# Kernel optimization log

Hardware: AMD Instinct MI355X
Metric: run time of the kernel (lower is better)

The kernel has to match this reference:

```python
import jax, jax.numpy as jnp
import numpy as np

B, K = 16, 256
APP, DK, DG, NR = 768, 96, 96, 8


def setup_inputs() -> dict:
    key = jax.random.key(0)
    ks = jax.random.split(key, 10)
    sA = 1.0 / np.sqrt(APP)  # torch Linear default init scale
    sG = 1.0 / np.sqrt(DG)
    return {
        "f_a": jax.random.normal(ks[0], (B, K, APP), jnp.float32),
        "position_embedding": jax.random.uniform(ks[1], (B, K, K, DG), jnp.float32),
        "WG_w": jax.random.normal(ks[2], (NR, DG), jnp.float32) * sG,
        "WG_b": jnp.zeros((NR,), jnp.float32),
        "WK_w": jax.random.normal(ks[3], (NR, DK, APP), jnp.float32) * sA,
        "WK_b": jnp.zeros((NR, DK), jnp.float32),
        "WQ_w": jax.random.normal(ks[4], (NR, DK, APP), jnp.float32) * sA,
        "WQ_b": jnp.zeros((NR, DK), jnp.float32),
        "WV_w": jax.random.normal(ks[5], (NR, DK, APP), jnp.float32) * sA,
        "WV_b": jnp.zeros((NR, DK), jnp.float32),
    }


def reference(f_a, position_embedding, WG_w, WG_b, WK_w, WK_b, WQ_w, WQ_b, WV_w, WV_b):
    # geometric bias: [NR, B, K, K]
    w_g = jax.nn.relu(jnp.einsum('bmng,rg->rbmn', position_embedding, WG_w)
                      + WG_b[:, None, None, None])
    # projections: [NR, B, K, DK]
    w_k = jnp.einsum('bmd,rkd->rbmk', f_a, WK_w) + WK_b[:, None, None, :]
    w_q = jnp.einsum('bnd,rkd->rbnk', f_a, WQ_w) + WQ_b[:, None, None, :]
    w_v = jnp.einsum('bmd,rkd->rbmk', f_a, WV_w) + WV_b[:, None, None, :]
    # scaled dot: scores[r,b,m,n] = <k_m, q_n>/sqrt(DK)
    scores = jnp.einsum('rbmk,rbnk->rbmn', w_k, w_q) / jnp.sqrt(jnp.float32(DK))
    logits = jnp.log(jnp.clip(w_g, 1e-6)) + scores
    # softmax over m (the key index, torch dim=1 of [B,K,K])
    att = jax.nn.softmax(logits, axis=2)
    # out[r,b,n,k] = sum_m att[r,b,m,n] * v[r,b,m,k]
    out = jnp.einsum('rbmn,rbmk->rbnk', att, w_v)
    # concat units along feature dim -> [B, K, NR*DK], residual add
    out = out.transpose(1, 2, 0, 3).reshape(B, K, NR * DK)
    return out + f_a
```

## Files before the change

### kernel.cpp

```cpp
#include <hip/hip_runtime.h>
#include <hip/hip_bf16.h>

typedef __attribute__((ext_vector_type(8))) short s16x8;
typedef __attribute__((ext_vector_type(4))) float f32x4;
typedef unsigned short u16;
typedef unsigned int u32;

#define NB 16
#define NK 256
#define APP 768
#define DKK 96
#define NR 8
#define QSCALE 0.10206207261596575f

__device__ __forceinline__ u16 f2bf(float f) {
  union { float f; unsigned int u; } v; v.f = f;
  unsigned int x = v.u;
  x += 0x7fffu + ((x >> 16) & 1u);
  return (u16)(x >> 16);
}
__device__ __forceinline__ float bf2f(u16 h) {
  union { unsigned int u; float f; } v; v.u = ((unsigned int)h) << 16;
  return v.f;
}
__device__ __forceinline__ u32 cvtpk(float lo, float hi) {
  u32 r;
  asm("v_cvt_pk_bf16_f32 %0, %1, %2" : "=v"(r) : "v"(lo), "v"(hi));
  return r;
}
__device__ __forceinline__ float bflo(u32 pk) {
  union { u32 u; float f; } v; v.u = pk << 16; return v.f;
}
__device__ __forceinline__ float bfhi(u32 pk) {
  union { u32 u; float f; } v; v.u = pk & 0xffff0000u; return v.f;
}
__device__ __forceinline__ void gload_lds16(const void* g, void* l) {
  __builtin_amdgcn_global_load_lds(
      (const __attribute__((address_space(1))) unsigned int*)g,
      (__attribute__((address_space(3))) unsigned int*)l, 16, 0, 0);
}

__global__ __launch_bounds__(256) void conv_kernel(
    const float* __restrict__ fa,
    const float* __restrict__ WKw, const float* __restrict__ WQw,
    const float* __restrict__ WVw,
    u16* __restrict__ fab, u16* __restrict__ Wb)
{
  const int idx = blockIdx.x * 256 + threadIdx.x;
  const int faCh = NB * NK * APP / 8;
  const int wCh  = NR * DKK * APP / 8;
  const float* src; u16* dst;
  if (idx < faCh) {
    src = fa + (size_t)idx * 8;
    dst = fab + (size_t)idx * 8;
  } else {
    int o = idx - faCh;
    int a = o / wCh;
    int oo = o - a * wCh;
    const float* wsrc = a == 0 ? WKw : (a == 1 ? WQw : WVw);
    src = wsrc + (size_t)oo * 8;
    dst = Wb + (size_t)a * (NR * DKK * APP) + (size_t)oo * 8;
  }
  float4 v0 = *(const float4*)src;
  float4 v1 = *(const float4*)(src + 4);
  s16x8 ov = {(short)f2bf(v0.x),(short)f2bf(v0.y),(short)f2bf(v0.z),(short)f2bf(v0.w),
              (short)f2bf(v1.x),(short)f2bf(v1.y),(short)f2bf(v1.z),(short)f2bf(v1.w)};
  *(s16x8*)dst = ov;
}

#define PROJ_BLKS 576
#define WG_BLKS 8192

__global__ __launch_bounds__(256) void fused_kernel(
    const u16* __restrict__ fab, const u16* __restrict__ Wb,
    const float* __restrict__ WKb, const float* __restrict__ WQb,
    const float* __restrict__ WVb,
    u16* __restrict__ wkF, u16* __restrict__ wqF, u16* __restrict__ wvF,
    const float* __restrict__ pos,
    const float* __restrict__ WGw, const float* __restrict__ WGb,
    u16* __restrict__ lb2)
{
  __shared__ u16 SH[26624];
  const int t = threadIdx.x;
  const int lane = t & 63, w = t >> 6;
  const int c = lane & 15, g = lane >> 4;
  const int bid = blockIdx.x;
  const int q = bid / 15, rph = bid - q * 15;

  if (rph == 0 && q < PROJ_BLKS) {
    u16* As = SH;
    u16* Bs = SH + 8192;
    const int pb = q;
    const int wr = w >> 1, wc = w & 1;
    const int m0 = (pb & 31) * 128;
    const int ct = pb >> 5;
    const int c0 = ct * 128;

    f32x4 acc[4][4] = {};

    for (int k0 = 0; k0 < APP; k0 += 64) {
      __syncthreads();
      #pragma unroll
      for (int i = 0; i < 4; ++i) {
        int n = t + i * 256;
        int row = n >> 3, cg = n & 7;
        int scg = cg ^ (row & 7);
        gload_lds16(fab + (size_t)(m0 + row) * APP + k0 + scg * 8, As + n * 8);
        gload_lds16(Wb  + (size_t)(c0 + row) * APP + k0 + scg * 8, Bs + n * 8);
      }
      __syncthreads();
      #pragma unroll
      for (int kc = 0; kc < 2; ++kc) {
        s16x8 af[4], bfr[4];
        #pragma unroll
        for (int i = 0; i < 4; ++i) {
          int arow = wr * 64 + i * 16 + c;
          af[i]  = *(const s16x8*)(As + (((arow << 3) | ((kc * 4 + g) ^ (arow & 7))) << 3));
          int brow = wc * 64 + i * 16 + c;
          bfr[i] = *(const s16x8*)(Bs + (((brow << 3) | ((kc * 4 + g) ^ (brow & 7))) << 3));
        }
        #pragma unroll
        for (int mi = 0; mi < 4; ++mi)
          #pragma unroll
          for (int ni = 0; ni < 4; ++ni)
            acc[mi][ni] = __builtin_amdgcn_mfma_f32_16x16x32_bf16(af[mi], bfr[ni], acc[mi][ni], 0, 0, 0);
      }
    }

    const int arr = ct / 6;
    const int cw0 = c0 - arr * APP;
    const float* bp = arr == 0 ? WKb : (arr == 1 ? WQb : WVb);

    #pragma unroll
    for (int mi = 0; mi < 4; ++mi)
      #pragma unroll
      for (int ni = 0; ni < 4; ++ni) {
        int clw = cw0 + wc * 64 + ni * 16 + c;
        float bias = bp[clw];
        int rr = clw / DKK, kk = clw - rr * DKK;
        int mb = m0 + wr * 64 + mi * 16 + g * 4;
        int bi = mb >> 8, tt = mb & 255;
        size_t hb = (size_t)rr * NB + bi;
        if (arr == 2) {
          ushort4 pk4;
          pk4.x = f2bf(acc[mi][ni][0] + bias);
          pk4.y = f2bf(acc[mi][ni][1] + bias);
          pk4.z = f2bf(acc[mi][ni][2] + bias);
          pk4.w = f2bf(acc[mi][ni][3] + bias);
          *(ushort4*)&wvF[((hb * 32 + (tt >> 3)) * DKK + kk) * 8 + (tt & 7)] = pk4;
        } else {
          u16* op = arr == 0 ? wkF : wqF;
          size_t base = ((hb * 12 + (kk >> 3)) * NK) * 8 + (size_t)(kk & 7);
          #pragma unroll
          for (int e = 0; e < 4; ++e) {
            float val = acc[mi][ni][e] + bias;
            if (arr == 1) val *= QSCALE;
            op[base + (size_t)(tt + e) * 8] = f2bf(val);
          }
        }
      }
  } else {
    const int nbefore = (q >= PROJ_BLKS) ? PROJ_BLKS : (q + (rph > 0 ? 1 : 0));
    const int wgid = bid - nbefore;
    u16* Th = SH;
    u16* Tl = SH + 13312;
    const size_t row0 = (size_t)wgid * 128;

    s16x8 bwh[3], bwl[3];
    #pragma unroll
    for (int kc = 0; kc < 3; ++kc) {
      const float* wp = WGw + (c & 7) * DKK + kc * 32 + g * 8;
      s16x8 hv, lv;
      #pragma unroll
      for (int j = 0; j < 4; ++j) {
        float x0 = wp[2 * j], x1 = wp[2 * j + 1];
        u32 h = cvtpk(x0, x1);
        u32 l = cvtpk(x0 - bflo(h), x1 - bfhi(h));
        hv[2 * j] = (short)(h & 0xffff); hv[2 * j + 1] = (short)(h >> 16);
        lv[2 * j] = (short)(l & 0xffff); lv[2 * j + 1] = (short)(l >> 16);
      }
      bwh[kc] = hv; bwl[kc] = lv;
    }
    const float bias = WGb[c & 7];

    #pragma unroll
    for (int i = 0; i < 6; ++i) {
      int qq = t + i * 256;
      int row = qq / 12, col8 = qq - row * 12;
      const float* s = pos + row0 * DKK + (size_t)qq * 8;
      float4 a = *(const float4*)s;
      float4 b = *(const float4*)(s + 4);
      uint4 ph, pl;
      ph.x = cvtpk(a.x, a.y); pl.x = cvtpk(a.x - bflo(ph.x), a.y - bfhi(ph.x));
      ph.y = cvtpk(a.z, a.w); pl.y = cvtpk(a.z - bflo(ph.y), a.w - bfhi(ph.y));
      ph.z = cvtpk(b.x, b.y); pl.z = cvtpk(b.x - bflo(ph.z), b.y - bfhi(ph.z));
      ph.w = cvtpk(b.z, b.w); pl.w = cvtpk(b.z - bflo(ph.w), b.w - bfhi(ph.w));
      *(uint4*)&Th[row * 104 + col8 * 8] = ph;
      *(uint4*)&Tl[row * 104 + col8 * 8] = pl;
    }
    __syncthreads();

    #pragma unroll
    for (int gi = 0; gi < 2; ++gi) {
      int rowl = w * 32 + gi * 16;
      f32x4 acc = {0.f, 0.f, 0.f, 0.f};
      #pragma unroll
      for (int kc = 0; kc < 3; ++kc) {
        s16x8 ah = *(const s16x8*)&Th[(rowl + c) * 104 + kc * 32 + g * 8];
        s16x8 al = *(const s16x8*)&Tl[(rowl + c) * 104 + kc * 32 + g * 8];
        acc = __builtin_amdgcn_mfma_f32_16x16x32_bf16(ah, bwh[kc], acc, 0, 0, 0);
        acc = __builtin_amdgcn_mfma_f32_16x16x32_bf16(ah, bwl[kc], acc, 0, 0, 0);
        acc = __builtin_amdgcn_mfma_f32_16x16x32_bf16(al, bwh[kc], acc, 0, 0, 0);
      }
      if (c < 8) {
        size_t base = (size_t)c * (NB * NK * NK) + row0 + rowl + g * 4;
        float v0 = __logf(fmaxf(acc[0] + bias, 1e-6f));
        float v1 = __logf(fmaxf(acc[1] + bias, 1e-6f));
        float v2 = __logf(fmaxf(acc[2] + bias, 1e-6f));
        float v3 = __logf(fmaxf(acc[3] + bias, 1e-6f));
        uint2 pk;
        pk.x = cvtpk(v0, v1);
        pk.y = cvtpk(v2, v3);
        *(uint2*)(lb2 + base) = pk;
      }
    }
  }
}

__global__ __launch_bounds__(256) void attn_kernel(
    const u16* __restrict__ wkF, const u16* __restrict__ wqF,
    const u16* __restrict__ wvF, const u16* __restrict__ lb2,
    const float* __restrict__ fa, float* __restrict__ out)
{
  __shared__ u16 Ps[4][16][40];
  const int t = threadIdx.x;
  const int w = t >> 6, lane = t & 63;
  const int c = lane & 15, g = lane >> 4;
  const int b = blockIdx.y, r = blockIdx.z;
  const int nb = blockIdx.x * 64 + w * 16;

  const size_t hb = (size_t)r * NB + b;
  const u16* Qb = wqF + hb * (12 * NK * 8);
  const u16* Kb = wkF + hb * (12 * NK * 8);
  const u16* Vb = wvF + hb * (32 * DKK * 8);
  const u16* Br = lb2 + hb * NK * NK + (size_t)c * NK + nb + g * 4;

  s16x8 qf[3];
  #pragma unroll
  for (int kc = 0; kc < 3; ++kc)
    qf[kc] = *(const s16x8*)(Qb + ((kc * 4 + g) * NK + nb + c) * 8);

  ushort4 bbr[16];
  #pragma unroll
  for (int mt = 0; mt < 16; ++mt)
    bbr[mt] = *(const ushort4*)(Br + (size_t)mt * 16 * NK);

  f32x4 S[16];
  #pragma unroll
  for (int mt = 0; mt < 16; ++mt) {
    f32x4 sa = {bf2f(bbr[mt].x), bf2f(bbr[mt].y), bf2f(bbr[mt].z), bf2f(bbr[mt].w)};
    #pragma unroll
    for (int kc = 0; kc < 3; ++kc) {
      s16x8 kf = *(const s16x8*)(Kb + ((kc * 4 + g) * NK + mt * 16 + c) * 8);
      sa = __builtin_amdgcn_mfma_f32_16x16x32_bf16(qf[kc], kf, sa, 0, 0, 0);
    }
    S[mt] = sa;
  }

  float rinv[4];
  #pragma unroll
  for (int e = 0; e < 4; ++e) {
    float mx = S[0][e];
    #pragma unroll
    for (int mt = 1; mt < 16; ++mt) mx = fmaxf(mx, S[mt][e]);
    mx = fmaxf(mx, __shfl_xor(mx, 1));
    mx = fmaxf(mx, __shfl_xor(mx, 2));
    mx = fmaxf(mx, __shfl_xor(mx, 4));
    mx = fmaxf(mx, __shfl_xor(mx, 8));
    float sm = 0.f;
    #pragma unroll
    for (int mt = 0; mt < 16; ++mt) {
      float p = __expf(S[mt][e] - mx);
      S[mt][e] = p;
      sm += p;
    }
    sm += __shfl_xor(sm, 1);
    sm += __shfl_xor(sm, 2);
    sm += __shfl_xor(sm, 4);
    sm += __shfl_xor(sm, 8);
    rinv[e] = 1.f / sm;
  }

  f32x4 o[6];
  #pragma unroll
  for (int ki = 0; ki < 6; ++ki) o[ki] = (f32x4){0.f, 0.f, 0.f, 0.f};

  #pragma unroll
  for (int mc = 0; mc < 8; ++mc) {
    #pragma unroll
    for (int e = 0; e < 4; ++e) {
      Ps[w][g * 4 + e][c]      = f2bf(S[2 * mc][e]);
      Ps[w][g * 4 + e][16 + c] = f2bf(S[2 * mc + 1][e]);
    }
    s16x8 pa = *(const s16x8*)&Ps[w][c][g * 8];
    #pragma unroll
    for (int ki = 0; ki < 6; ++ki) {
      s16x8 vf = *(const s16x8*)(Vb + ((mc * 4 + g) * DKK + ki * 16 + c) * 8);
      o[ki] = __builtin_amdgcn_mfma_f32_16x16x32_bf16(pa, vf, o[ki], 0, 0, 0);
    }
  }

  #pragma unroll
  for (int ki = 0; ki < 6; ++ki)
    #pragma unroll
    for (int e = 0; e < 4; ++e) {
      int n = nb + g * 4 + e;
      size_t adr = ((size_t)b * NK + n) * (NR * DKK) + r * DKK + ki * 16 + c;
      out[adr] = o[ki][e] * rinv[e] + fa[adr];
    }
}

extern "C" void kernel_launch(void* const* d_in, const int* in_sizes, int n_in,
                              void* d_out, int out_size, void* d_ws, size_t ws_size,
                              hipStream_t stream) {
  (void)in_sizes; (void)n_in; (void)out_size; (void)ws_size;
  const float* fa  = (const float*)d_in[0];
  const float* pos = (const float*)d_in[1];
  const float* WGw = (const float*)d_in[2];
  const float* WGb = (const float*)d_in[3];
  const float* WKw = (const float*)d_in[4];
  const float* WKb = (const float*)d_in[5];
  const float* WQw = (const float*)d_in[6];
  const float* WQb = (const float*)d_in[7];
  const float* WVw = (const float*)d_in[8];
  const float* WVb = (const float*)d_in[9];
  float* outp = (float*)d_out;

  const size_t faN = (size_t)NB * NK * APP;
  const size_t wN  = (size_t)3 * NR * DKK * APP;
  const size_t kqv = (size_t)NR * NB * NK * DKK;
  u16* fab = (u16*)d_ws;
  u16* Wb  = fab + faN;
  u16* wkF = Wb + wN;
  u16* wqF = wkF + kqv;
  u16* wvF = wqF + kqv;
  u16* lb2 = wvF + kqv;

  hipLaunchKernelGGL(conv_kernel, dim3(2400), dim3(256), 0, stream,
                     fa, WKw, WQw, WVw, fab, Wb);
  hipLaunchKernelGGL(fused_kernel, dim3(PROJ_BLKS + WG_BLKS), dim3(256), 0, stream,
                     fab, Wb, WKb, WQb, WVb, wkF, wqF, wvF, pos, WGw, WGb, lb2);
  hipLaunchKernelGGL(attn_kernel, dim3(4, NB, NR), dim3(256), 0, stream,
                     wkF, wqF, wvF, lb2, fa, outp);
}
```

Measured before the change: 137.4 us.

## Make geometric-bias blocks persistent with double-buffered register prefetch

The geometric-bias part of the fused kernel now uses 2304 persistent blocks that loop over 16384 tiles of 64 rows, instead of 8192 one-shot blocks of 128 rows. Each iteration prefetches the next tile's position embeddings into registers while the MFMA work on the current LDS buffer runs, then writes the split bf16 hi/lo values into the other LDS buffer. The interleave with projection blocks changes from one in every 15 blocks to one in every 5, for 2880 blocks total. The aim is to hide global load latency on the memory-bound position-embedding stream and cut block launch overhead, at the cost of more live registers and a barrier on every tile.

Result: no change. 134.8 us (-1.8%).

```diff
diff --git a/kernel.cpp b/kernel.cpp
--- a/kernel.cpp
+++ b/kernel.cpp
@@ -69,7 +69,8 @@
 }
 
 #define PROJ_BLKS 576
-#define WG_BLKS 8192
+#define WG_BLKS 2304
+#define NTILES 16384
 
 __global__ __launch_bounds__(256) void fused_kernel(
     const u16* __restrict__ fab, const u16* __restrict__ Wb,
@@ -85,9 +86,9 @@
   const int lane = t & 63, w = t >> 6;
   const int c = lane & 15, g = lane >> 4;
   const int bid = blockIdx.x;
-  const int q = bid / 15, rph = bid - q * 15;
-
-  if (rph == 0 && q < PROJ_BLKS) {
+  const int q = bid / 5, rem = bid - q * 5;
+
+  if (rem == 0) {
     u16* As = SH;
     u16* Bs = SH + 8192;
     const int pb = q;
@@ -160,11 +161,7 @@
         }
       }
   } else {
-    const int nbefore = (q >= PROJ_BLKS) ? PROJ_BLKS : (q + (rph > 0 ? 1 : 0));
-    const int wgid = bid - nbefore;
-    u16* Th = SH;
-    u16* Tl = SH + 13312;
-    const size_t row0 = (size_t)wgid * 128;
+    const int wgid = q * 4 + rem - 1;
 
     s16x8 bwh[3], bwl[3];
     #pragma unroll
@@ -183,46 +180,102 @@
     }
     const float bias = WGb[c & 7];
 
-    #pragma unroll
-    for (int i = 0; i < 6; ++i) {
-      int qq = t + i * 256;
-      int row = qq / 12, col8 = qq - row * 12;
-      const float* s = pos + row0 * DKK + (size_t)qq * 8;
-      float4 a = *(const float4*)s;
-      float4 b = *(const float4*)(s + 4);
-      uint4 ph, pl;
-      ph.x = cvtpk(a.x, a.y); pl.x = cvtpk(a.x - bflo(ph.x), a.y - bfhi(ph.x));
-      ph.y = cvtpk(a.z, a.w); pl.y = cvtpk(a.z - bflo(ph.y), a.w - bfhi(ph.y));
-      ph.z = cvtpk(b.x, b.y); pl.z = cvtpk(b.x - bflo(ph.z), b.y - bfhi(ph.z));
-      ph.w = cvtpk(b.z, b.w); pl.w = cvtpk(b.z - bflo(ph.w), b.w - bfhi(ph.w));
-      *(uint4*)&Th[row * 104 + col8 * 8] = ph;
-      *(uint4*)&Tl[row * 104 + col8 * 8] = pl;
+    const int qq0 = t, qq1 = t + 256, qq2 = t + 512;
+    const int r0 = qq0 / 12, c8_0 = qq0 - r0 * 12;
+    const int r1 = qq1 / 12, c8_1 = qq1 - r1 * 12;
+    const int r2 = qq2 / 12, c8_2 = qq2 - r2 * 12;
+    const int ld0 = r0 * 104 + c8_0 * 8;
+    const int ld1 = r1 * 104 + c8_1 * 8;
+    const int ld2 = r2 * 104 + c8_2 * 8;
+    const int rowl = w * 16;
+
+    float4 la0, lb0, la1, lb1, la2, lb2v;
+
+    int tile = wgid;
+    {
+      const float* s0 = pos + (size_t)tile * 6144 + (size_t)qq0 * 8;
+      const float* s1 = pos + (size_t)tile * 6144 + (size_t)qq1 * 8;
+      const float* s2 = pos + (size_t)tile * 6144 + (size_t)qq2 * 8;
+      la0 = *(const float4*)s0; lb0 = *(const float4*)(s0 + 4);
+      la1 = *(const float4*)s1; lb1 = *(const float4*)(s1 + 4);
+      la2 = *(const float4*)s2; lb2v = *(const float4*)(s2 + 4);
+    }
+    {
+      u16* Th = SH;
+      u16* Tl = SH + 6656;
+      #pragma unroll
+      for (int i = 0; i < 3; ++i) {
+        float4 a = i == 0 ? la0 : (i == 1 ? la1 : la2);
+        float4 b = i == 0 ? lb0 : (i == 1 ? lb1 : lb2v);
+        int off = i == 0 ? ld0 : (i == 1 ? ld1 : ld2);
+        uint4 ph, pl;
+        ph.x = cvtpk(a.x, a.y); pl.x = cvtpk(a.x - bflo(ph.x), a.y - bfhi(ph.x));
+        ph.y = cvtpk(a.z, a.w); pl.y = cvtpk(a.z - bflo(ph.y), a.w - bfhi(ph.y));
+        ph.z = cvtpk(b.x, b.y); pl.z = cvtpk(b.x - bflo(ph.z), b.y - bfhi(ph.z));
+        ph.w = cvtpk(b.z, b.w); pl.w = cvtpk(b.z - bflo(ph.w), b.w - bfhi(ph.w));
+        *(uint4*)&Th[off] = ph;
+        *(uint4*)&Tl[off] = pl;
+      }
     }
     __syncthreads();
 
-    #pragma unroll
-    for (int gi = 0; gi < 2; ++gi) {
-      int rowl = w * 32 + gi * 16;
-      f32x4 acc = {0.f, 0.f, 0.f, 0.f};
-      #pragma unroll
-      for (int kc = 0; kc < 3; ++kc) {
-        s16x8 ah = *(const s16x8*)&Th[(rowl + c) * 104 + kc * 32 + g * 8];
-        s16x8 al = *(const s16x8*)&Tl[(rowl + c) * 104 + kc * 32 + g * 8];
-        acc = __builtin_amdgcn_mfma_f32_16x16x32_bf16(ah, bwh[kc], acc, 0, 0, 0);
-        acc = __builtin_amdgcn_mfma_f32_16x16x32_bf16(ah, bwl[kc], acc, 0, 0, 0);
-        acc = __builtin_amdgcn_mfma_f32_16x16x32_bf16(al, bwh[kc], acc, 0, 0, 0);
-      }
-      if (c < 8) {
-        size_t base = (size_t)c * (NB * NK * NK) + row0 + rowl + g * 4;
-        float v0 = __logf(fmaxf(acc[0] + bias, 1e-6f));
-        float v1 = __logf(fmaxf(acc[1] + bias, 1e-6f));
-        float v2 = __logf(fmaxf(acc[2] + bias, 1e-6f));
-        float v3 = __logf(fmaxf(acc[3] + bias, 1e-6f));
-        uint2 pk;
-        pk.x = cvtpk(v0, v1);
-        pk.y = cvtpk(v2, v3);
-        *(uint2*)(lb2 + base) = pk;
-      }
+    int cur = 0;
+    while (true) {
+      const int nxt = tile + WG_BLKS;
+      const bool more = (nxt < NTILES);
+      if (more) {
+        const float* s0 = pos + (size_t)nxt * 6144 + (size_t)qq0 * 8;
+        const float* s1 = pos + (size_t)nxt * 6144 + (size_t)qq1 * 8;
+        const float* s2 = pos + (size_t)nxt * 6144 + (size_t)qq2 * 8;
+        la0 = *(const float4*)s0; lb0 = *(const float4*)(s0 + 4);
+        la1 = *(const float4*)s1; lb1 = *(const float4*)(s1 + 4);
+        la2 = *(const float4*)s2; lb2v = *(const float4*)(s2 + 4);
+      }
+      {
+        const u16* Th = SH + (cur ? 13312 : 0);
+        const u16* Tl = Th + 6656;
+        f32x4 acc = {0.f, 0.f, 0.f, 0.f};
+        #pragma unroll
+        for (int kc = 0; kc < 3; ++kc) {
+          s16x8 ah = *(const s16x8*)&Th[(rowl + c) * 104 + kc * 32 + g * 8];
+          s16x8 al = *(const s16x8*)&Tl[(rowl + c) * 104 + kc * 32 + g * 8];
+          acc = __builtin_amdgcn_mfma_f32_16x16x32_bf16(ah, bwh[kc], acc, 0, 0, 0);
+          acc = __builtin_amdgcn_mfma_f32_16x16x32_bf16(ah, bwl[kc], acc, 0, 0, 0);
+          acc = __builtin_amdgcn_mfma_f32_16x16x32_bf16(al, bwh[kc], acc, 0, 0, 0);
+        }
+        if (c < 8) {
+          size_t base = (size_t)c * (NB * NK * NK) + (size_t)tile * 64 + rowl + g * 4;
+          float v0 = __logf(fmaxf(acc[0] + bias, 1e-6f));
+          float v1 = __logf(fmaxf(acc[1] + bias, 1e-6f));
+          float v2 = __logf(fmaxf(acc[2] + bias, 1e-6f));
+          float v3 = __logf(fmaxf(acc[3] + bias, 1e-6f));
+          uint2 pk;
+          pk.x = cvtpk(v0, v1);
+          pk.y = cvtpk(v2, v3);
+          *(uint2*)(lb2 + base) = pk;
+        }
+      }
+      if (!more) break;
+      {
+        u16* Th = SH + (cur ? 0 : 13312);
+        u16* Tl = Th + 6656;
+        #pragma unroll
+        for (int i = 0; i < 3; ++i) {
+          float4 a = i == 0 ? la0 : (i == 1 ? la1 : la2);
+          float4 b = i == 0 ? lb0 : (i == 1 ? lb1 : lb2v);
+          int off = i == 0 ? ld0 : (i == 1 ? ld1 : ld2);
+          uint4 ph, pl;
+          ph.x = cvtpk(a.x, a.y); pl.x = cvtpk(a.x - bflo(ph.x), a.y - bfhi(ph.x));
+          ph.y = cvtpk(a.z, a.w); pl.y = cvtpk(a.z - bflo(ph.y), a.w - bfhi(ph.y));
+          ph.z = cvtpk(b.x, b.y); pl.z = cvtpk(b.x - bflo(ph.z), b.y - bfhi(ph.z));
+          ph.w = cvtpk(b.z, b.w); pl.w = cvtpk(b.z - bflo(ph.w), b.w - bfhi(ph.w));
+          *(uint4*)&Th[off] = ph;
+          *(uint4*)&Tl[off] = pl;
+        }
+      }
+      __syncthreads();
+      cur ^= 1;
+      tile = nxt;
     }
   }
 }
@@ -348,7 +401,7 @@
 
   hipLaunchKernelGGL(conv_kernel, dim3(2400), dim3(256), 0, stream,
                      fa, WKw, WQw, WVw, fab, Wb);
-  hipLaunchKernelGGL(fused_kernel, dim3(PROJ_BLKS + WG_BLKS), dim3(256), 0, stream,
+  hipLaunchKernelGGL(fused_kernel, dim3((PROJ_BLKS + WG_BLKS) * 5 / 5 == 0 ? 2880 : 2880), dim3(256), 0, stream,
                      fab, Wb, WKb, WQb, WVb, wkF, wqF, wvF, pos, WGw, WGb, lb2);
   hipLaunchKernelGGL(attn_kernel, dim3(4, NB, NR), dim3(256), 0, stream,
                      wkF, wqF, wvF, lb2, fa, outp);
```
